# Performance work log

Hardware: AMD Instinct MI355X
Metric: run time of the kernel (lower is better)

The kernel has to match this reference:

```python
import jax, jax.numpy as jnp
import numpy as np


def setup_inputs() -> dict:
    key = jax.random.key(0)
    k1, k2, k3 = jax.random.split(key, 3)
    x = jax.random.normal(k1, (8192, 4096), dtype=jnp.float32)
    # int8 quantized weight codes (stored as int32 per harness dtypes)
    q_layer = jax.random.randint(k2, (4096, 4096), 0, 127, dtype=jnp.int32)
    weight_scale = jax.random.uniform(k3, (1,), dtype=jnp.float32)
    return {"x": x, "q_layer": q_layer, "weight_scale": weight_scale}


def reference(x, q_layer, weight_scale):
    # Dequantize: cast int codes to fp32, multiply by scalar scale.
    W_approx = q_layer.astype(jnp.float32) * weight_scale  # [out, in]
    # F.linear(x, W) = x @ W.T
    return jnp.einsum('bi,oi->bo', x, W_approx)
```

## Files before the change

kernel.cpp:

```cpp
#include <hip/hip_runtime.h>


typedef unsigned short u16;
typedef __attribute__((ext_vector_type(4))) int int4v;
typedef __attribute__((ext_vector_type(4))) float float4v;

constexpr int Mdim = 8192, Ndim = 4096, Kdim = 4096;
constexpr int BM = 256, BN = 256, BK = 64;
constexpr int NT_N = Ndim / BN;
constexpr int NWG = (Mdim / BM) * (Ndim / BN);
constexpr int NTILES = Kdim / BK;

#define GLOAD16(gp, lp)                                                      \
  __builtin_amdgcn_global_load_lds(                                          \
      (const __attribute__((address_space(1))) void*)(gp),                   \
      (__attribute__((address_space(3))) void*)(lp), 16, 0, 0)
#define FENCE() asm volatile("" ::: "memory")
#define BARRIER()                      \
  do {                                 \
    FENCE();                           \
    __builtin_amdgcn_s_barrier();      \
    FENCE();                           \
  } while (0)
#define WAIT_VM(n) asm volatile("s_waitcnt vmcnt(" #n ")" ::: "memory")

__global__ void quant_x_i8(const float* __restrict__ x,
                           signed char* __restrict__ xq,
                           float* __restrict__ sr) {
  const int row = blockIdx.x;
  const int t = threadIdx.x;
  const float4v* px = (const float4v*)(x + (size_t)row * Kdim);
  float4v v[4];
  float am = 0.f;
#pragma unroll
  for (int i = 0; i < 4; ++i) {
    v[i] = px[t * 4 + i];
#pragma unroll
    for (int j = 0; j < 4; ++j) am = fmaxf(am, fabsf(v[i][j]));
  }
#pragma unroll
  for (int off = 32; off; off >>= 1) am = fmaxf(am, __shfl_xor(am, off));
  __shared__ float wm[4];
  if ((t & 63) == 0) wm[t >> 6] = am;
  __syncthreads();
  am = fmaxf(fmaxf(wm[0], wm[1]), fmaxf(wm[2], wm[3]));
  const float rcp = am > 0.f ? 127.0f / am : 0.f;
  if (t == 0) sr[row] = am * (1.0f / 127.0f);
  int o[4];
#pragma unroll
  for (int i = 0; i < 4; ++i) {
    int q0 = __float2int_rn(v[i][0] * rcp);
    int q1 = __float2int_rn(v[i][1] * rcp);
    int q2 = __float2int_rn(v[i][2] * rcp);
    int q3 = __float2int_rn(v[i][3] * rcp);
    o[i] = (q0 & 255) | ((q1 & 255) << 8) | ((q2 & 255) << 16) | (q3 << 24);
  }
  int4v ov = {o[0], o[1], o[2], o[3]};
  ((int4v*)(xq + (size_t)row * Kdim))[t] = ov;
}

__global__ void cvt_q_i8(const int* __restrict__ q,
                         signed char* __restrict__ qq, int n16) {
  int i = blockIdx.x * blockDim.x + threadIdx.x;
  const int stride = gridDim.x * blockDim.x;
  for (; i < n16; i += stride) {
    const int4v* p = (const int4v*)q + i * 4;
    int o[4];
#pragma unroll
    for (int k = 0; k < 4; ++k) {
      int4v w = p[k];
      o[k] = w[0] | (w[1] << 8) | (w[2] << 16) | (w[3] << 24);
    }
    int4v ov = {o[0], o[1], o[2], o[3]};
    ((int4v*)qq)[i] = ov;
  }
}

__global__ __launch_bounds__(512, 2) void gemm_i8(
    const signed char* __restrict__ A, const signed char* __restrict__ B,
    float* __restrict__ C, const float* __restrict__ srow,
    const float* __restrict__ scale_p) {
  __shared__ signed char sA[3][BM * BK];
  __shared__ signed char sB[3][BN * BK];

  const int tid = threadIdx.x;
  const int wid = tid >> 6, lane = tid & 63;
  const int fr = lane & 15;
  const int kg = lane >> 4;
  const int kx = ((kg ^ ((fr >> 1) & 3)) << 4);

  const int bid = blockIdx.x;
  const int swz = (bid & 7) * (NWG / 8) + (bid >> 3);
  const int mt = swz / NT_N, ntl = swz % NT_N;
  const int brow = mt * BM, bcol = ntl * BN;

  const int wm = wid >> 2, wn = wid & 3;

  const int strow = wid * 16 + (lane >> 2);
  const int stcol = (((lane & 3) ^ ((lane >> 3) & 3)) << 4);
  const signed char* gA[2];
  const signed char* gB[2];
#pragma unroll
  for (int j = 0; j < 2; ++j) {
    gA[j] = A + (size_t)(brow + j * 128 + strow) * Kdim + stcol;
    gB[j] = B + (size_t)(bcol + j * 128 + strow) * Kdim + stcol;
  }

  auto stage4 = [&](int slot, int t) {
#pragma unroll
    for (int j = 0; j < 2; ++j)
      GLOAD16(gA[j] + t * BK, &sA[slot][j * 8192 + wid * 1024]);
#pragma unroll
    for (int j = 0; j < 2; ++j)
      GLOAD16(gB[j] + t * BK, &sB[slot][j * 8192 + wid * 1024]);
  };
  auto loadA = [&](int4v* af, int sl, int ch) {
#pragma unroll
    for (int m = 0; m < 4; ++m)
      af[m] = *(const int4v*)(const void*)&sA[sl]
                  [(wm * 128 + ch * 64 + m * 16 + fr) * BK + kx];
  };
  auto loadB = [&](int4v* bf, int sl) {
#pragma unroll
    for (int n = 0; n < 4; ++n)
      bf[n] = *(const int4v*)(const void*)&sB[sl]
                  [(wn * 64 + n * 16 + fr) * BK + kx];
  };

  int4v acc[2][4][4] = {};

  auto mma16 = [&](int ch, const int4v* af, const int4v* bf) {
    __builtin_amdgcn_s_setprio(1);
#pragma unroll
    for (int m = 0; m < 4; ++m)
#pragma unroll
      for (int n = 0; n < 4; ++n)
        acc[ch][m][n] = __builtin_amdgcn_mfma_i32_16x16x64_i8(
            af[m], bf[n], acc[ch][m][n], 0, 0, 0);
    __builtin_amdgcn_s_setprio(0);
  };

  stage4(0, 0);
  stage4(1, 1);
  WAIT_VM(4);
  BARRIER();

#pragma unroll 3
  for (int u = 0; u < NTILES; ++u) {
    const int sl = u % 3;
    const int st = (u + 2) % 3;
    const int t2 = (u + 2 < NTILES) ? u + 2 : NTILES - 1;
    int4v a[4], b[4];

    loadB(b, sl);
    loadA(a, sl, 0);
    stage4(st, t2);
    BARRIER();
    mma16(0, a, b);
    BARRIER();

    loadA(a, sl, 1);
    BARRIER();
    mma16(1, a, b);
    WAIT_VM(4);
    BARRIER();
  }

  WAIT_VM(0);
  BARRIER();

  const float sw = *scale_p;
  const int col0 = bcol + wn * 64 + fr;
  const int rb = (lane >> 4) * 4;
#pragma unroll
  for (int ch = 0; ch < 2; ++ch)
#pragma unroll
    for (int m = 0; m < 4; ++m)
#pragma unroll
      for (int j = 0; j < 4; ++j) {
        const int row = brow + wm * 128 + ch * 64 + m * 16 + rb + j;
        const float f = srow[row] * sw;
#pragma unroll
        for (int n = 0; n < 4; ++n)
          C[(size_t)row * Ndim + (col0 + n * 16)] =
              (float)acc[ch][m][n][j] * f;
      }
}

extern "C" void kernel_launch(void* const* d_in, const int* in_sizes, int n_in,
                              void* d_out, int out_size, void* d_ws,
                              size_t ws_size, hipStream_t stream) {
  const float* x = (const float*)d_in[0];
  const int* q = (const int*)d_in[1];
  const float* scale = (const float*)d_in[2];
  float* out = (float*)d_out;

  signed char* xq = (signed char*)d_ws;
  signed char* qq = xq + (size_t)Mdim * Kdim;
  float* sr = (float*)(qq + (size_t)Ndim * Kdim);
  const size_t ws_needed =
      (size_t)Mdim * Kdim + (size_t)Ndim * Kdim + Mdim * sizeof(float);
  if (ws_size < ws_needed) return;

  quant_x_i8<<<Mdim, 256, 0, stream>>>(x, xq, sr);
  cvt_q_i8<<<2048, 256, 0, stream>>>(q, qq, (Ndim * Kdim) / 16);
  gemm_i8<<<NWG, 512, 0, stream>>>(xq, qq, out, sr, scale);
}
```

Measured before the change: 198.6 us.

## Deepen LDS ring to four stages and double-buffer MFMA fragments in registers

```diff
diff --git a/kernel.cpp b/kernel.cpp
--- a/kernel.cpp
+++ b/kernel.cpp
@@ -1,7 +1,6 @@
 #include <hip/hip_runtime.h>
 
 
-typedef unsigned short u16;
 typedef __attribute__((ext_vector_type(4))) int int4v;
 typedef __attribute__((ext_vector_type(4))) float float4v;
 
@@ -80,8 +79,8 @@
     const signed char* __restrict__ A, const signed char* __restrict__ B,
     float* __restrict__ C, const float* __restrict__ srow,
     const float* __restrict__ scale_p) {
-  __shared__ signed char sA[3][BM * BK];
-  __shared__ signed char sB[3][BN * BK];
+  __shared__ signed char sA[4][BM * BK];
+  __shared__ signed char sB[4][BN * BK];
 
   const int tid = threadIdx.x;
   const int wid = tid >> 6, lane = tid & 63;
@@ -114,60 +113,68 @@
     for (int j = 0; j < 2; ++j)
       GLOAD16(gB[j] + t * BK, &sB[slot][j * 8192 + wid * 1024]);
   };
-  auto loadA = [&](int4v* af, int sl, int ch) {
-#pragma unroll
-    for (int m = 0; m < 4; ++m)
-      af[m] = *(const int4v*)(const void*)&sA[sl]
-                  [(wm * 128 + ch * 64 + m * 16 + fr) * BK + kx];
-  };
-  auto loadB = [&](int4v* bf, int sl) {
+  auto loadA8 = [&](int4v* af, int sl) {
+#pragma unroll
+    for (int ch = 0; ch < 2; ++ch)
+#pragma unroll
+      for (int m = 0; m < 4; ++m)
+        af[ch * 4 + m] = *(const int4v*)(const void*)&sA[sl]
+                             [(wm * 128 + ch * 64 + m * 16 + fr) * BK + kx];
+  };
+  auto loadB4 = [&](int4v* bf, int sl) {
 #pragma unroll
     for (int n = 0; n < 4; ++n)
       bf[n] = *(const int4v*)(const void*)&sB[sl]
                   [(wn * 64 + n * 16 + fr) * BK + kx];
   };
 
-  int4v acc[2][4][4] = {};
-
-  auto mma16 = [&](int ch, const int4v* af, const int4v* bf) {
+  int4v acc[8][4] = {};
+
+  auto mma32 = [&](const int4v* af, const int4v* bf) {
     __builtin_amdgcn_s_setprio(1);
 #pragma unroll
-    for (int m = 0; m < 4; ++m)
-#pragma unroll
-      for (int n = 0; n < 4; ++n)
-        acc[ch][m][n] = __builtin_amdgcn_mfma_i32_16x16x64_i8(
-            af[m], bf[n], acc[ch][m][n], 0, 0, 0);
+    for (int ch = 0; ch < 2; ++ch)
+#pragma unroll
+      for (int m = 0; m < 4; ++m)
+#pragma unroll
+        for (int n = 0; n < 4; ++n)
+          acc[ch * 4 + m][n] = __builtin_amdgcn_mfma_i32_16x16x64_i8(
+              af[ch * 4 + m], bf[n], acc[ch * 4 + m][n], 0, 0, 0);
     __builtin_amdgcn_s_setprio(0);
+  };
+
+  int4v aE[8], bE[4], aO[8], bO[4];
+
+  auto body = [&](int u, const int4v* aC, const int4v* bC, int4v* aN,
+                  int4v* bN) {
+    const int su1 = (u + 1) & 3;
+    const int st3 = (u + 3) & 3;
+    const int t3 = (u + 3 < NTILES) ? u + 3 : NTILES - 1;
+    loadB4(bN, su1);
+    loadA8(aN, su1);
+    stage4(st3, t3);
+    mma32(aC, bC);
+    WAIT_VM(4);
+    BARRIER();
   };
 
   stage4(0, 0);
   stage4(1, 1);
+  stage4(2, 2);
+  WAIT_VM(8);
+  BARRIER();
+  loadB4(bE, 0);
+  loadA8(aE, 0);
   WAIT_VM(4);
   BARRIER();
 
-#pragma unroll 3
-  for (int u = 0; u < NTILES; ++u) {
-    const int sl = u % 3;
-    const int st = (u + 2) % 3;
-    const int t2 = (u + 2 < NTILES) ? u + 2 : NTILES - 1;
-    int4v a[4], b[4];
-
-    loadB(b, sl);
-    loadA(a, sl, 0);
-    stage4(st, t2);
-    BARRIER();
-    mma16(0, a, b);
-    BARRIER();
-
-    loadA(a, sl, 1);
-    BARRIER();
-    mma16(1, a, b);
-    WAIT_VM(4);
-    BARRIER();
+#pragma unroll 2
+  for (int u = 0; u < NTILES; u += 2) {
+    body(u, aE, bE, aO, bO);
+    body(u + 1, aO, bO, aE, bE);
   }
 
   WAIT_VM(0);
-  BARRIER();
 
   const float sw = *scale_p;
   const int col0 = bcol + wn * 64 + fr;
@@ -183,7 +190,7 @@
 #pragma unroll
         for (int n = 0; n < 4; ++n)
           C[(size_t)row * Ndim + (col0 + n * 16)] =
-              (float)acc[ch][m][n][j] * f;
+              (float)acc[ch * 4 + m][n][j] * f;
       }
 }
 
```

New measurement: 192.1 us. 3.2% less time.
